# Optimization experiments

Hardware: AMD Instinct MI355X
Metric: run time of the kernel (lower is better)

The kernel has to match this reference:

```python
import jax, jax.numpy as jnp
import numpy as np

N_NODES = 100000
N_EDGES = 1200000
IN_CH = 64
HID = 64
OUT_CH = 8
N_GRAPHS = 256


def setup_inputs() -> dict:
    key = jax.random.key(0)
    ks = jax.random.split(key, 12)
    x = jax.random.normal(ks[0], (N_NODES, IN_CH), dtype=jnp.float32)
    edge_index = jax.random.randint(ks[1], (2, N_EDGES), 0, N_NODES, dtype=jnp.int64)
    batch = jnp.sort(jax.random.randint(ks[2], (N_NODES,), 0, N_GRAPHS, dtype=jnp.int64))
    s1 = 1.0 / np.sqrt(IN_CH)
    s2 = 1.0 / np.sqrt(HID)
    # SAGEConv: lin_l (aggregated neighbors, with bias), lin_r (root, no bias)
    W1l = jax.random.uniform(ks[3], (HID, IN_CH), jnp.float32, -s1, s1)
    b1l = jax.random.uniform(ks[4], (HID,), jnp.float32, -s1, s1)
    W1r = jax.random.uniform(ks[5], (HID, IN_CH), jnp.float32, -s1, s1)
    W2l = jax.random.uniform(ks[6], (HID, HID), jnp.float32, -s2, s2)
    b2l = jax.random.uniform(ks[7], (HID,), jnp.float32, -s2, s2)
    W2r = jax.random.uniform(ks[8], (HID, HID), jnp.float32, -s2, s2)
    Wc = jax.random.uniform(ks[9], (OUT_CH, HID), jnp.float32, -s2, s2)
    bc = jax.random.uniform(ks[10], (OUT_CH,), jnp.float32, -s2, s2)
    return {"x": x, "edge_index": edge_index, "batch": batch,
            "W1l": W1l, "b1l": b1l, "W1r": W1r,
            "W2l": W2l, "b2l": b2l, "W2r": W2r,
            "Wc": Wc, "bc": bc}


def _sage_conv(x, src, dst, Wl, bl, Wr):
    # mean aggregation of neighbor (source) features onto targets
    agg = jax.ops.segment_sum(x[src], dst, num_segments=x.shape[0])  # [N, d]
    cnt = jax.ops.segment_sum(jnp.ones((src.shape[0],), x.dtype), dst,
                              num_segments=x.shape[0])
    agg = agg / jnp.maximum(cnt, 1.0)[:, None]
    return agg @ Wl.T + bl + x @ Wr.T


def reference(x, edge_index, batch, W1l, b1l, W1r, W2l, b2l, W2r, Wc, bc):
    src, dst = edge_index[0], edge_index[1]
    h = jax.nn.relu(_sage_conv(x, src, dst, W1l, b1l, W1r))
    # dropout p=0.2 is identity in eval mode
    h = jax.nn.relu(_sage_conv(h, src, dst, W2l, b2l, W2r))
    # global mean pool over graphs
    gsum = jax.ops.segment_sum(h, batch, num_segments=N_GRAPHS)      # [G, HID]
    gcnt = jax.ops.segment_sum(jnp.ones((h.shape[0],), h.dtype), batch,
                               num_segments=N_GRAPHS)
    g = gsum / jnp.maximum(gcnt, 1.0)[:, None]
    return g @ Wc.T + bc
```

## Files before the change

kernel.cpp:

```cpp
#include <hip/hip_runtime.h>

#define N_NODES 100000
#define N_EDGES 1200000
#define CH 64
#define NG 256
#define OC 8
#define NBUK 196
#define BINCHUNK 4096
#define NBLKA 293
#define NSTRIP 6250

typedef unsigned short ushort_t;
typedef unsigned int uint_t;
typedef __attribute__((ext_vector_type(8))) short bf16x8;
typedef __attribute__((ext_vector_type(4))) float f32x4;

__device__ __forceinline__ ushort_t f2bf(float f) {
  uint_t u = __float_as_uint(f);
  return (ushort_t)((u + 0x7FFFu + ((u >> 16) & 1u)) >> 16);
}
__device__ __forceinline__ float bfE(uint_t u) {
  return __uint_as_float(u << 16);
}
__device__ __forceinline__ float bfO(uint_t u) {
  return __uint_as_float(u & 0xFFFF0000u);
}

__global__ __launch_bounds__(256) void countA_k(const int* __restrict__ dst,
                                                int* __restrict__ gbase) {
  __shared__ int hist[NBUK];
  for (int i = threadIdx.x; i < NBUK; i += 256) hist[i] = 0;
  __syncthreads();
  const int cs = blockIdx.x * BINCHUNK;
  int ce = cs + BINCHUNK;
  if (ce > N_EDGES) ce = N_EDGES;
  for (int e = cs + threadIdx.x; e < ce; e += 256)
    atomicAdd(&hist[dst[e] >> 9], 1);
  __syncthreads();
  for (int b = threadIdx.x; b < NBUK; b += 256) {
    int c = hist[b];
    if (c) atomicAdd(&gbase[b], c);
  }
}

__global__ void scanB_k(const int* __restrict__ gbase, int* __restrict__ boff,
                        int* __restrict__ cursor) {
  __shared__ int s[256];
  int v = (threadIdx.x < NBUK) ? gbase[threadIdx.x] : 0;
  s[threadIdx.x] = v;
  __syncthreads();
  for (int o = 1; o < 256; o <<= 1) {
    int t = (threadIdx.x >= o) ? s[threadIdx.x - o] : 0;
    __syncthreads();
    s[threadIdx.x] += t;
    __syncthreads();
  }
  if (threadIdx.x < NBUK) {
    int ex = s[threadIdx.x] - v;
    boff[threadIdx.x] = ex;
    cursor[threadIdx.x] = ex;
  }
  if (threadIdx.x == NBUK - 1) boff[NBUK] = s[threadIdx.x];
}

__global__ __launch_bounds__(256) void scatterA_k(const int* __restrict__ src,
                                                  const int* __restrict__ dst,
                                                  int* __restrict__ cursor,
                                                  int* __restrict__ tmp) {
  __shared__ int hist[NBUK];
  for (int i = threadIdx.x; i < NBUK; i += 256) hist[i] = 0;
  __syncthreads();
  const int cs = blockIdx.x * BINCHUNK;
  int ce = cs + BINCHUNK;
  if (ce > N_EDGES) ce = N_EDGES;
  for (int e = cs + threadIdx.x; e < ce; e += 256)
    atomicAdd(&hist[dst[e] >> 9], 1);
  __syncthreads();
  for (int b = threadIdx.x; b < NBUK; b += 256) {
    int c = hist[b];
    hist[b] = c ? atomicAdd(&cursor[b], c) : 0;
  }
  __syncthreads();
  for (int e = cs + threadIdx.x; e < ce; e += 256) {
    int d = dst[e];
    int slot = atomicAdd(&hist[d >> 9], 1);
    tmp[slot] = (src[e] << 9) | (d & 511);
  }
}

__global__ __launch_bounds__(512) void csrC_k(const int* __restrict__ tmp,
                                              const int* __restrict__ boff,
                                              int* __restrict__ rp,
                                              int* __restrict__ col) {
  __shared__ int lh[512];
  __shared__ int s[512];
  const int b = blockIdx.x;
  const int tid = threadIdx.x;
  const int eb = boff[b], ee = boff[b + 1];
  lh[tid] = 0;
  __syncthreads();
  for (int e = eb + tid; e < ee; e += 512) atomicAdd(&lh[tmp[e] & 511], 1);
  __syncthreads();
  int v = lh[tid];
  s[tid] = v;
  __syncthreads();
  for (int o = 1; o < 512; o <<= 1) {
    int t = (tid >= o) ? s[tid - o] : 0;
    __syncthreads();
    s[tid] += t;
    __syncthreads();
  }
  const int base = eb + s[tid] - v;
  const int node = b * 512 + tid;
  if (node < N_NODES) rp[node] = base;
  if (b == 0 && tid == 0) rp[N_NODES] = N_EDGES;
  lh[tid] = base;
  __syncthreads();
  for (int e = eb + tid; e < ee; e += 512) {
    int p = tmp[e];
    int slot = atomicAdd(&lh[p & 511], 1);
    col[slot] = p >> 9;
  }
}

template <typename TIN>
__global__ __launch_bounds__(256) void transform_mfma_k(
    const TIN* __restrict__ in, const float* __restrict__ Wl,
    const float* __restrict__ Wr, ushort_t* __restrict__ outl,
    ushort_t* __restrict__ outr) {
  const int wid = blockIdx.x * 4 + (threadIdx.x >> 6);
  if (wid >= NSTRIP) return;
  const int lane = threadIdx.x & 63;
  const int row = lane & 15;
  const int kb = lane >> 4;

  bf16x8 Bfrag[8][2];
#pragma unroll
  for (int t = 0; t < 8; ++t) {
    const float* W = (t < 4) ? Wl : Wr;
    const int j = (t & 3) * 16 + row;
#pragma unroll
    for (int h = 0; h < 2; ++h) {
      const float* p = W + j * CH + h * 32 + kb * 8;
      float4 w0 = *(const float4*)p;
      float4 w1 = *(const float4*)(p + 4);
      bf16x8 b;
      b[0] = (short)f2bf(w0.x); b[1] = (short)f2bf(w0.y);
      b[2] = (short)f2bf(w0.z); b[3] = (short)f2bf(w0.w);
      b[4] = (short)f2bf(w1.x); b[5] = (short)f2bf(w1.y);
      b[6] = (short)f2bf(w1.z); b[7] = (short)f2bf(w1.w);
      Bfrag[t][h] = b;
    }
  }

  const int n0 = wid * 16;
  bf16x8 Afrag[2];
#pragma unroll
  for (int h = 0; h < 2; ++h) {
    if constexpr (sizeof(TIN) == 4) {
      const float* p = (const float*)in + (size_t)(n0 + row) * CH + h * 32 + kb * 8;
      float4 a0 = *(const float4*)p;
      float4 a1 = *(const float4*)(p + 4);
      bf16x8 a;
      a[0] = (short)f2bf(a0.x); a[1] = (short)f2bf(a0.y);
      a[2] = (short)f2bf(a0.z); a[3] = (short)f2bf(a0.w);
      a[4] = (short)f2bf(a1.x); a[5] = (short)f2bf(a1.y);
      a[6] = (short)f2bf(a1.z); a[7] = (short)f2bf(a1.w);
      Afrag[h] = a;
    } else {
      const ushort_t* p = (const ushort_t*)in + (size_t)(n0 + row) * CH + h * 32 + kb * 8;
      Afrag[h] = *(const bf16x8*)p;
    }
  }

  f32x4 acc[8];
#pragma unroll
  for (int t = 0; t < 8; ++t) {
    acc[t] = (f32x4){0.f, 0.f, 0.f, 0.f};
    acc[t] = __builtin_amdgcn_mfma_f32_16x16x32_bf16(Afrag[0], Bfrag[t][0],
                                                     acc[t], 0, 0, 0);
    acc[t] = __builtin_amdgcn_mfma_f32_16x16x32_bf16(Afrag[1], Bfrag[t][1],
                                                     acc[t], 0, 0, 0);
  }

  const int orow = (lane >> 4) * 4;
#pragma unroll
  for (int t = 0; t < 4; ++t)
#pragma unroll
    for (int i = 0; i < 4; ++i)
      outl[(size_t)(n0 + orow + i) * CH + t * 16 + row] = f2bf(acc[t][i]);
#pragma unroll
  for (int t = 4; t < 8; ++t)
#pragma unroll
    for (int i = 0; i < 4; ++i)
      outr[(size_t)(n0 + orow + i) * CH + (t - 4) * 16 + row] = f2bf(acc[t][i]);
}

template <int MODE>
__global__ __launch_bounds__(256) void gather_k(
    const uint_t* __restrict__ glu, const uint_t* __restrict__ gru,
    const float* __restrict__ bl, const int* __restrict__ rowptr,
    const int* __restrict__ col, uint_t* __restrict__ outu,
    const int* __restrict__ batch, float* __restrict__ gsum,
    int* __restrict__ gcnt) {
  const int lane = threadIdx.x & 63;
  const int half = lane >> 5;
  const int cp = lane & 31;
  const float bE = bl[2 * cp], bO = bl[2 * cp + 1];
  const int wid = blockIdx.x * (blockDim.x >> 6) + (threadIdx.x >> 6);
  const int nw = gridDim.x * (blockDim.x >> 6);
  const int per = (N_NODES + nw - 1) / nw;
  int ns = wid * per;
  int ne = ns + per;
  if (ne > N_NODES) ne = N_NODES;
  if (ns >= ne) return;

  int curg = -1;
  float paccE = 0.f, paccO = 0.f;
  int pcnt = 0;

  for (int n = ns; n < ne; ++n) {
    const int eb = rowptr[n], ee = rowptr[n + 1];
    float e0 = 0.f, o0 = 0.f, e1 = 0.f, o1 = 0.f;
    float e2 = 0.f, o2 = 0.f, e3 = 0.f, o3 = 0.f;
    int j = eb + half;
    for (; j + 6 < ee; j += 8) {
      int c0 = col[j], c1 = col[j + 2], c4 = col[j + 4], c6 = col[j + 6];
      uint_t u0 = glu[(size_t)c0 * 32 + cp];
      uint_t u1 = glu[(size_t)c1 * 32 + cp];
      uint_t u2 = glu[(size_t)c4 * 32 + cp];
      uint_t u3 = glu[(size_t)c6 * 32 + cp];
      e0 += bfE(u0); o0 += bfO(u0);
      e1 += bfE(u1); o1 += bfO(u1);
      e2 += bfE(u2); o2 += bfO(u2);
      e3 += bfE(u3); o3 += bfO(u3);
    }
    for (; j < ee; j += 2) {
      uint_t u = glu[(size_t)col[j] * 32 + cp];
      e0 += bfE(u); o0 += bfO(u);
    }
    float sE = (e0 + e1) + (e2 + e3);
    float sO = (o0 + o1) + (o2 + o3);
    sE += __shfl_xor(sE, 32);
    sO += __shfl_xor(sO, 32);
    const int deg = ee - eb;
    const float inv = deg > 0 ? 1.f / (float)deg : 1.f;
    const uint_t ug = gru[(size_t)n * 32 + cp];
    const float rE = fmaxf(fmaf(sE, inv, bE + bfE(ug)), 0.f);
    const float rO = fmaxf(fmaf(sO, inv, bO + bfO(ug)), 0.f);
    if (MODE == 0) {
      if (half == 0)
        outu[(size_t)n * 32 + cp] = ((uint_t)f2bf(rO) << 16) | f2bf(rE);
    } else {
      int g = batch[n];
      if (g != curg) {
        if (curg >= 0 && half == 0) {
          atomicAdd(&gsum[curg * CH + 2 * cp], paccE);
          atomicAdd(&gsum[curg * CH + 2 * cp + 1], paccO);
          if (lane == 0) atomicAdd(&gcnt[curg], pcnt);
        }
        curg = g;
        paccE = 0.f;
        paccO = 0.f;
        pcnt = 0;
      }
      paccE += rE;
      paccO += rO;
      pcnt++;
    }
  }
  if (MODE == 1 && curg >= 0 && half == 0) {
    atomicAdd(&gsum[curg * CH + 2 * cp], paccE);
    atomicAdd(&gsum[curg * CH + 2 * cp + 1], paccO);
    if (lane == 0) atomicAdd(&gcnt[curg], pcnt);
  }
}

__global__ void final_k(const float* __restrict__ gsum, const int* __restrict__ gcnt,
                        const float* __restrict__ Wc, const float* __restrict__ bc,
                        float* __restrict__ out) {
  __shared__ float Wcs[OC * CH];
  __shared__ float bcs[OC];
  for (int i = threadIdx.x; i < OC * CH; i += blockDim.x) Wcs[i] = Wc[i];
  if (threadIdx.x < OC) bcs[threadIdx.x] = bc[threadIdx.x];
  __syncthreads();
  int g = threadIdx.x;
  float c = (float)gcnt[g];
  float inv = c > 0.f ? 1.f / c : 1.f;
  float gr[CH];
#pragma unroll
  for (int k = 0; k < CH; ++k) gr[k] = gsum[g * CH + k] * inv;
#pragma unroll
  for (int o = 0; o < OC; ++o) {
    float acc = bcs[o];
#pragma unroll
    for (int k = 0; k < CH; ++k) acc += gr[k] * Wcs[o * CH + k];
    out[g * OC + o] = acc;
  }
}

extern "C" void kernel_launch(void* const* d_in, const int* in_sizes, int n_in,
                              void* d_out, int out_size, void* d_ws, size_t ws_size,
                              hipStream_t stream) {
  const float* x   = (const float*)d_in[0];
  const int*   ei  = (const int*)d_in[1];
  const int*   bat = (const int*)d_in[2];
  const float* W1l = (const float*)d_in[3];
  const float* b1l = (const float*)d_in[4];
  const float* W1r = (const float*)d_in[5];
  const float* W2l = (const float*)d_in[6];
  const float* b2l = (const float*)d_in[7];
  const float* W2r = (const float*)d_in[8];
  const float* Wc  = (const float*)d_in[9];
  const float* bc  = (const float*)d_in[10];
  float* out = (float*)d_out;

  char* ws = (char*)d_ws;
  ushort_t* buf1 = (ushort_t*)(ws + 0);
  ushort_t* buf3 = (ushort_t*)(ws + 12800000);
  ushort_t* buf2 = (ushort_t*)(ws + 25600000);
  int*   tmp     = (int*)(ws + 0);
  int*   rp      = (int*)(ws + 51200000);
  int*   col     = (int*)(ws + 51600128);
  int*   gbase   = (int*)(ws + 56400128);
  int*   boff    = (int*)(ws + 56401152);
  int*   cursor  = (int*)(ws + 56402176);
  float* gsum    = (float*)(ws + 56403200);
  int*   gcnt    = (int*)(ws + 56468736);

  const int* src = ei;
  const int* dst = ei + N_EDGES;

  hipMemsetAsync(gbase, 0, NBUK * sizeof(int), stream);
  hipMemsetAsync(gsum, 0, (size_t)NG * CH * sizeof(float) + NG * sizeof(int), stream);

  countA_k<<<NBLKA, 256, 0, stream>>>(dst, gbase);
  scanB_k<<<1, 256, 0, stream>>>(gbase, boff, cursor);
  scatterA_k<<<NBLKA, 256, 0, stream>>>(src, dst, cursor, tmp);
  csrC_k<<<NBUK, 512, 0, stream>>>(tmp, boff, rp, col);

  transform_mfma_k<float><<<(NSTRIP + 3) / 4, 256, 0, stream>>>(x, W1l, W1r,
                                                                buf1, buf2);
  gather_k<0><<<2048, 256, 0, stream>>>((const uint_t*)buf1, (const uint_t*)buf2,
                                        b1l, rp, col, (uint_t*)buf3,
                                        nullptr, nullptr, nullptr);
  transform_mfma_k<ushort_t><<<(NSTRIP + 3) / 4, 256, 0, stream>>>(buf3, W2l, W2r,
                                                                   buf1, buf2);
  gather_k<1><<<2048, 256, 0, stream>>>((const uint_t*)buf1, (const uint_t*)buf2,
                                        b2l, rp, col, nullptr,
                                        bat, gsum, gcnt);
  final_k<<<1, 256, 0, stream>>>(gsum, gcnt, Wc, bc, out);
}
```

Baseline: 235.5 us.

## Shard features into 8-channel slices and gather per slice with edge-parallel lanes

Intermediate bf16 feature buffers move from row-major [N,64] to eight channel-sliced planes of [N,8], each holding 16 bytes per node. Each gather block handles one slice, chosen from blockIdx, so a slice's working set is about 1.6MB and can stay cache-resident. Within a wave, 16 edges are processed in parallel with 4 lanes per edge, and the partial sums are combined with xor shuffles. The cost is 8x more passes over col/rowptr, smaller 16-byte random accesses, and more shuffle reductions per node; the transform's stores and second-layer loads become strided.

Measured after the change: 595.1 us. +152.7%, slower.

```diff
diff --git a/kernel.cpp b/kernel.cpp
--- a/kernel.cpp
+++ b/kernel.cpp
@@ -9,6 +9,8 @@
 #define BINCHUNK 4096
 #define NBLKA 293
 #define NSTRIP 6250
+#define SHU 400000
+#define SHS 800000
 
 typedef unsigned short ushort_t;
 typedef unsigned int uint_t;
@@ -168,7 +170,8 @@
       a[6] = (short)f2bf(a1.z); a[7] = (short)f2bf(a1.w);
       Afrag[h] = a;
     } else {
-      const ushort_t* p = (const ushort_t*)in + (size_t)(n0 + row) * CH + h * 32 + kb * 8;
+      const ushort_t* p =
+          (const ushort_t*)in + (size_t)(h * 4 + kb) * SHS + (size_t)(n0 + row) * 8;
       Afrag[h] = *(const bf16x8*)p;
     }
   }
@@ -185,15 +188,21 @@
 
   const int orow = (lane >> 4) * 4;
 #pragma unroll
-  for (int t = 0; t < 4; ++t)
+  for (int t = 0; t < 4; ++t) {
+    const int ch = t * 16 + row;
+    ushort_t* po = outl + (size_t)(ch >> 3) * SHS + (ch & 7);
 #pragma unroll
     for (int i = 0; i < 4; ++i)
-      outl[(size_t)(n0 + orow + i) * CH + t * 16 + row] = f2bf(acc[t][i]);
-#pragma unroll
-  for (int t = 4; t < 8; ++t)
+      po[(size_t)(n0 + orow + i) * 8] = f2bf(acc[t][i]);
+  }
+#pragma unroll
+  for (int t = 4; t < 8; ++t) {
+    const int ch = (t - 4) * 16 + row;
+    ushort_t* po = outr + (size_t)(ch >> 3) * SHS + (ch & 7);
 #pragma unroll
     for (int i = 0; i < 4; ++i)
-      outr[(size_t)(n0 + orow + i) * CH + (t - 4) * 16 + row] = f2bf(acc[t][i]);
+      po[(size_t)(n0 + orow + i) * 8] = f2bf(acc[t][i]);
+  }
 }
 
 template <int MODE>
@@ -203,14 +212,17 @@
     const int* __restrict__ col, uint_t* __restrict__ outu,
     const int* __restrict__ batch, float* __restrict__ gsum,
     int* __restrict__ gcnt) {
+  const int s = blockIdx.x & 7;
+  const uint_t* gls = glu + (size_t)s * SHU;
+  const uint_t* grs = gru + (size_t)s * SHU;
   const int lane = threadIdx.x & 63;
-  const int half = lane >> 5;
-  const int cp = lane & 31;
-  const float bE = bl[2 * cp], bO = bl[2 * cp + 1];
-  const int wid = blockIdx.x * (blockDim.x >> 6) + (threadIdx.x >> 6);
-  const int nw = gridDim.x * (blockDim.x >> 6);
-  const int per = (N_NODES + nw - 1) / nw;
-  int ns = wid * per;
+  const int d = lane & 3;
+  const int eg = lane >> 2;
+  const float bE = bl[s * 8 + 2 * d];
+  const float bO = bl[s * 8 + 2 * d + 1];
+  const int chunk = (blockIdx.x >> 3) * 4 + (threadIdx.x >> 6);
+  const int per = 196;
+  int ns = chunk * per;
   int ne = ns + per;
   if (ne > N_NODES) ne = N_NODES;
   if (ns >= ne) return;
@@ -218,46 +230,43 @@
   int curg = -1;
   float paccE = 0.f, paccO = 0.f;
   int pcnt = 0;
+  int eb = rowptr[ns];
 
   for (int n = ns; n < ne; ++n) {
-    const int eb = rowptr[n], ee = rowptr[n + 1];
-    float e0 = 0.f, o0 = 0.f, e1 = 0.f, o1 = 0.f;
-    float e2 = 0.f, o2 = 0.f, e3 = 0.f, o3 = 0.f;
-    int j = eb + half;
-    for (; j + 6 < ee; j += 8) {
-      int c0 = col[j], c1 = col[j + 2], c4 = col[j + 4], c6 = col[j + 6];
-      uint_t u0 = glu[(size_t)c0 * 32 + cp];
-      uint_t u1 = glu[(size_t)c1 * 32 + cp];
-      uint_t u2 = glu[(size_t)c4 * 32 + cp];
-      uint_t u3 = glu[(size_t)c6 * 32 + cp];
-      e0 += bfE(u0); o0 += bfO(u0);
-      e1 += bfE(u1); o1 += bfO(u1);
-      e2 += bfE(u2); o2 += bfO(u2);
-      e3 += bfE(u3); o3 += bfO(u3);
-    }
-    for (; j < ee; j += 2) {
-      uint_t u = glu[(size_t)col[j] * 32 + cp];
-      e0 += bfE(u); o0 += bfO(u);
-    }
-    float sE = (e0 + e1) + (e2 + e3);
-    float sO = (o0 + o1) + (o2 + o3);
-    sE += __shfl_xor(sE, 32);
-    sO += __shfl_xor(sO, 32);
+    const int ee = rowptr[n + 1];
     const int deg = ee - eb;
+    float aE = 0.f, aO = 0.f;
+    for (int g0 = eb; g0 < ee; g0 += 16) {
+      int eidx = g0 + eg;
+      if (eidx < ee) {
+        int c = col[eidx];
+        uint_t v = gls[(size_t)c * 4 + d];
+        aE += bfE(v);
+        aO += bfO(v);
+      }
+    }
+#pragma unroll
+    for (int o = 4; o <= 32; o <<= 1) {
+      aE += __shfl_xor(aE, o);
+      aO += __shfl_xor(aO, o);
+    }
     const float inv = deg > 0 ? 1.f / (float)deg : 1.f;
-    const uint_t ug = gru[(size_t)n * 32 + cp];
-    const float rE = fmaxf(fmaf(sE, inv, bE + bfE(ug)), 0.f);
-    const float rO = fmaxf(fmaf(sO, inv, bO + bfO(ug)), 0.f);
+    const uint_t ug = grs[(size_t)n * 4 + d];
+    const float rE = fmaxf(fmaf(aE, inv, bE + bfE(ug)), 0.f);
+    const float rO = fmaxf(fmaf(aO, inv, bO + bfO(ug)), 0.f);
     if (MODE == 0) {
-      if (half == 0)
-        outu[(size_t)n * 32 + cp] = ((uint_t)f2bf(rO) << 16) | f2bf(rE);
+      if (lane < 4)
+        outu[(size_t)s * SHU + (size_t)n * 4 + d] =
+            ((uint_t)f2bf(rO) << 16) | f2bf(rE);
     } else {
       int g = batch[n];
       if (g != curg) {
-        if (curg >= 0 && half == 0) {
-          atomicAdd(&gsum[curg * CH + 2 * cp], paccE);
-          atomicAdd(&gsum[curg * CH + 2 * cp + 1], paccO);
-          if (lane == 0) atomicAdd(&gcnt[curg], pcnt);
+        if (curg >= 0) {
+          if (lane < 4) {
+            atomicAdd(&gsum[curg * CH + s * 8 + 2 * d], paccE);
+            atomicAdd(&gsum[curg * CH + s * 8 + 2 * d + 1], paccO);
+          }
+          if (s == 0 && lane == 0) atomicAdd(&gcnt[curg], pcnt);
         }
         curg = g;
         paccE = 0.f;
@@ -268,11 +277,14 @@
       paccO += rO;
       pcnt++;
     }
-  }
-  if (MODE == 1 && curg >= 0 && half == 0) {
-    atomicAdd(&gsum[curg * CH + 2 * cp], paccE);
-    atomicAdd(&gsum[curg * CH + 2 * cp + 1], paccO);
-    if (lane == 0) atomicAdd(&gcnt[curg], pcnt);
+    eb = ee;
+  }
+  if (MODE == 1 && curg >= 0) {
+    if (lane < 4) {
+      atomicAdd(&gsum[curg * CH + s * 8 + 2 * d], paccE);
+      atomicAdd(&gsum[curg * CH + s * 8 + 2 * d + 1], paccO);
+    }
+    if (s == 0 && lane == 0) atomicAdd(&gcnt[curg], pcnt);
   }
 }
 
@@ -341,12 +353,12 @@
 
   transform_mfma_k<float><<<(NSTRIP + 3) / 4, 256, 0, stream>>>(x, W1l, W1r,
                                                                 buf1, buf2);
-  gather_k<0><<<2048, 256, 0, stream>>>((const uint_t*)buf1, (const uint_t*)buf2,
+  gather_k<0><<<1024, 256, 0, stream>>>((const uint_t*)buf1, (const uint_t*)buf2,
                                         b1l, rp, col, (uint_t*)buf3,
                                         nullptr, nullptr, nullptr);
   transform_mfma_k<ushort_t><<<(NSTRIP + 3) / 4, 256, 0, stream>>>(buf3, W2l, W2r,
                                                                    buf1, buf2);
-  gather_k<1><<<2048, 256, 0, stream>>>((const uint_t*)buf1, (const uint_t*)buf2,
+  gather_k<1><<<1024, 256, 0, stream>>>((const uint_t*)buf1, (const uint_t*)buf2,
                                         b2l, rp, col, nullptr,
                                         bat, gsum, gcnt);
   final_k<<<1, 256, 0, stream>>>(gsum, gcnt, Wc, bc, out);
```
